# Kernel optimization log

Measured on AMD Instinct MI355X. Metric: run time of the kernel, lower is better.

The kernel has to match this reference:

```python
import jax, jax.numpy as jnp
import numpy as np

B, T, D, H = 4, 2048, 1024, 16
HD = D // H  # head_dim = 64

def setup_inputs() -> dict:
    key = jax.random.key(0)
    k1, k2, k3 = jax.random.split(key, 3)
    s = 1.0 / np.sqrt(D)
    x = jax.random.normal(k1, (B, T, D), dtype=jnp.float32)
    W_qkv = jax.random.normal(k2, (D, 3 * D), dtype=jnp.float32) * s
    W_proj = jax.random.normal(k3, (D, D), dtype=jnp.float32) * s
    return {"x": x, "W_qkv": W_qkv, "W_proj": W_proj}

def reference(x, W_qkv, W_proj):
    Bq, Tq, C = x.shape
    qkv = x @ W_qkv                                   # [B,T,3C]
    q, k, v = jnp.split(qkv, 3, axis=-1)
    def heads(t):  # [B,T,C] -> [B,H,T,HD]
        return t.reshape(Bq, Tq, H, HD).transpose(0, 2, 1, 3)
    q, k, v = heads(q), heads(k), heads(v)
    scale = 1.0 / np.sqrt(HD)
    att = jnp.einsum('bhqd,bhkd->bhqk', q, k) * scale  # [B,H,T,T]
    causal = jnp.tril(jnp.ones((Tq, Tq), dtype=bool))
    att = jnp.where(causal[None, None], att, -jnp.inf)
    att = jax.nn.softmax(att, axis=-1)
    y = jnp.einsum('bhqk,bhkd->bhqd', att, v)          # [B,H,T,HD]
    y = y.transpose(0, 2, 1, 3).reshape(Bq, Tq, C)
    return y @ W_proj
```

## Files before the change

kernel.cpp:

```cpp
#include <hip/hip_runtime.h>

typedef unsigned short ushort_t;
typedef __attribute__((ext_vector_type(8))) __bf16 bf16x8;
typedef __attribute__((ext_vector_type(4))) float f32x4;
typedef __attribute__((ext_vector_type(16))) float f32x16;
typedef __attribute__((ext_vector_type(4))) float float4v;
typedef __attribute__((ext_vector_type(8))) unsigned short ushort8v;
typedef __attribute__((ext_vector_type(4))) unsigned short ushort4v;
typedef __attribute__((ext_vector_type(4))) unsigned uint4v;

#define T_LEN 2048
#define D_DIM 1024
#define NHEAD 16
#define HDIM 64
#define BH 64
#define MROWS 8192
#define PERQKV ((size_t)BH * T_LEN * HDIM)

__device__ __forceinline__ ushort_t f2bf(float f) {
  unsigned u = __builtin_bit_cast(unsigned, f);
  u = (u + 0x7FFFu + ((u >> 16) & 1u)) >> 16;
  return (ushort_t)u;
}

__device__ __forceinline__ float fast_exp2(float x) {
  float r; asm("v_exp_f32 %0, %1" : "=v"(r) : "v"(x)); return r;
}
__device__ __forceinline__ float fast_rcp(float x) {
  float r; asm("v_rcp_f32 %0, %1" : "=v"(r) : "v"(x)); return r;
}

__device__ __forceinline__ void load_lds16(const ushort_t* g, ushort_t* l) {
  __builtin_amdgcn_global_load_lds((const __attribute__((address_space(1))) void*)g,
                                   (__attribute__((address_space(3))) void*)l, 16, 0, 0);
}

__global__ __launch_bounds__(256) void k_prep(const float* __restrict__ x,
                                              const float* __restrict__ Wqkv,
                                              const float* __restrict__ Wproj,
                                              ushort_t* __restrict__ xb,
                                              ushort_t* __restrict__ WqT,
                                              ushort_t* __restrict__ WpT) {
  __shared__ ushort_t tile[32][33];
  int bid = blockIdx.x, tid = threadIdx.x;
  if (bid < 8192) {
    int i = bid * 256 + tid;
    float4v v = ((const float4v*)x)[i];
    ushort4v o;
    o[0] = f2bf(v[0]); o[1] = f2bf(v[1]); o[2] = f2bf(v[2]); o[3] = f2bf(v[3]);
    ((ushort4v*)xb)[i] = o;
    return;
  }
  bid -= 8192;
  int bx = bid & 127, by = bid >> 7;
  const float* W; ushort_t* Wt; int C;
  if (bx < 96) { W = Wqkv; Wt = WqT; C = 3072; }
  else         { W = Wproj; Wt = WpT; C = 1024; bx -= 96; }
  const int R = 1024;
  int tx = tid & 31, ty = tid >> 5;
  int r0 = by << 5, c0 = bx << 5;
#pragma unroll
  for (int i = 0; i < 4; ++i) {
    int r = ty + i * 8;
    tile[r][tx] = f2bf(W[(size_t)(r0 + r) * C + c0 + tx]);
  }
  __syncthreads();
#pragma unroll
  for (int i = 0; i < 4; ++i) {
    int r = ty + i * 8;
    Wt[(size_t)(c0 + r) * R + r0 + tx] = tile[tx][r];
  }
}

template <int N, int K, int EPI>
__global__ __launch_bounds__(256) void k_gemm(const ushort_t* __restrict__ A,
                                              const ushort_t* __restrict__ Bt,
                                              ushort_t* __restrict__ O16,
                                              float* __restrict__ O32) {
  __shared__ __align__(16) ushort_t Atile[128 * 32];
  __shared__ __align__(16) ushort_t Btile[128 * 32];
  const int tid = threadIdx.x;
  const int lane = tid & 63, w = tid >> 6;
  const int g = lane >> 4, c = lane & 15;
  const int wm = w >> 1, wn = w & 1;
  const int m0 = blockIdx.y * 128, n0 = blockIdx.x * 128;

  f32x4 acc[4][4];
#pragma unroll
  for (int i = 0; i < 4; ++i)
#pragma unroll
    for (int j = 0; j < 4; ++j) acc[i][j] = (f32x4){0.f, 0.f, 0.f, 0.f};

  for (int k0 = 0; k0 < K; k0 += 32) {
    __syncthreads();
#pragma unroll
    for (int r = 0; r < 2; ++r) {
      int flat = r * 256 + tid;
      int row = flat >> 2, slot = flat & 3;
      int gsl = slot ^ (row & 3);
      load_lds16(A + (size_t)(m0 + row) * K + k0 + gsl * 8,
                 &Atile[(r * 256 + w * 64) * 8]);
      load_lds16(Bt + (size_t)(n0 + row) * K + k0 + gsl * 8,
                 &Btile[(r * 256 + w * 64) * 8]);
    }
    __syncthreads();

    bf16x8 af[4], bfr[4];
#pragma unroll
    for (int mi = 0; mi < 4; ++mi) {
      int row = wm * 64 + mi * 16 + c;
      int sl = g ^ (row & 3);
      af[mi] = *(const bf16x8*)&Atile[row * 32 + sl * 8];
    }
#pragma unroll
    for (int ni = 0; ni < 4; ++ni) {
      int row = wn * 64 + ni * 16 + c;
      int sl = g ^ (row & 3);
      bfr[ni] = *(const bf16x8*)&Btile[row * 32 + sl * 8];
    }
#pragma unroll
    for (int mi = 0; mi < 4; ++mi)
#pragma unroll
      for (int ni = 0; ni < 4; ++ni)
        acc[mi][ni] = __builtin_amdgcn_mfma_f32_16x16x32_bf16(af[mi], bfr[ni],
                                                              acc[mi][ni], 0, 0, 0);
  }

#pragma unroll
  for (int mi = 0; mi < 4; ++mi)
#pragma unroll
    for (int ni = 0; ni < 4; ++ni) {
      int n = n0 + wn * 64 + ni * 16 + c;
#pragma unroll
      for (int j = 0; j < 4; ++j) {
        int m = m0 + wm * 64 + mi * 16 + g * 4 + j;
        float v = acc[mi][ni][j];
        if constexpr (EPI == 0) {
          int which = n >> 10, hn = n & 1023;
          int h = hn >> 6, d = hn & 63;
          int b = m >> 11, t = m & 2047;
          if (which == 0) v *= 0.18033688f;
          O16[(size_t)which * PERQKV +
              (((size_t)(b * NHEAD + h) * T_LEN + t) * HDIM + d)] = f2bf(v);
        } else {
          O32[(size_t)m * N + n] = v;
        }
      }
    }
}

template <int NB_TILES, int EPI>
__global__ __launch_bounds__(512, 2) void k_gemm3(const ushort_t* __restrict__ A,
                                                  const ushort_t* __restrict__ Bt,
                                                  ushort_t* __restrict__ O16,
                                                  float* __restrict__ O32) {
  __shared__ __align__(16) ushort_t As[3][128 * 64];
  __shared__ __align__(16) ushort_t Bs[3][256 * 64];
  const int tid = threadIdx.x, lane = tid & 63, w = tid >> 6;
  const int g = lane >> 4, c = lane & 15;
  const int wm = w & 1, wn = w >> 1;
  const int nblk = 64 * NB_TILES;
  const int chunk = nblk >> 3;
  const int bid = blockIdx.x;
  const int logical = (bid & 7) * chunk + (bid >> 3);
  const int mb = logical & 63, nb = logical >> 6;
  const int m0 = mb * 128, n0 = nb * 256;

  const int srow = lane >> 3, sgran = lane & 7;

  auto stage = [&](int t, int buf) {
    const int k0 = t * 64;
#pragma unroll
    for (int l = 0; l < 2; ++l) {
      int r = w * 16 + l * 8 + srow;
      load_lds16(A + (size_t)(m0 + r) * 1024 + k0 + ((sgran ^ (r & 7)) << 3),
                 &As[buf][(w * 16 + l * 8) * 64]);
    }
#pragma unroll
    for (int l = 0; l < 4; ++l) {
      int r = w * 32 + l * 8 + srow;
      load_lds16(Bt + (size_t)(n0 + r) * 1024 + k0 + ((sgran ^ (r & 7)) << 3),
                 &Bs[buf][(w * 32 + l * 8) * 64]);
    }
  };

  f32x4 acc[4][4];
#pragma unroll
  for (int i = 0; i < 4; ++i)
#pragma unroll
    for (int j = 0; j < 4; ++j) acc[i][j] = (f32x4){0.f, 0.f, 0.f, 0.f};

  stage(0, 0);
  stage(1, 1);

  for (int t = 0; t < 16; ++t) {
    if (t < 15) asm volatile("s_waitcnt vmcnt(6)" ::: "memory");
    else        asm volatile("s_waitcnt vmcnt(0)" ::: "memory");
    __builtin_amdgcn_s_barrier();
    __builtin_amdgcn_sched_barrier(0);

    if (t + 2 < 16) stage(t + 2, (t + 2) % 3);

    const int cur = t % 3;
    const ushort_t* abuf = &As[cur][0];
    const ushort_t* bbuf = &Bs[cur][0];
#pragma unroll
    for (int kk = 0; kk < 2; ++kk) {
      bf16x8 af[4], bq[4];
#pragma unroll
      for (int fr = 0; fr < 4; ++fr) {
        int r = wm * 64 + fr * 16 + c;
        af[fr] = *(const bf16x8*)&abuf[r * 64 + (((kk * 4 + g) ^ (r & 7)) << 3)];
      }
#pragma unroll
      for (int fc = 0; fc < 4; ++fc) {
        int r = wn * 64 + fc * 16 + c;
        bq[fc] = *(const bf16x8*)&bbuf[r * 64 + (((kk * 4 + g) ^ (r & 7)) << 3)];
      }
      __builtin_amdgcn_s_setprio(1);
#pragma unroll
      for (int fr = 0; fr < 4; ++fr)
#pragma unroll
        for (int fc = 0; fc < 4; ++fc)
          acc[fr][fc] = __builtin_amdgcn_mfma_f32_16x16x32_bf16(af[fr], bq[fc],
                                                                acc[fr][fc], 0, 0, 0);
      __builtin_amdgcn_s_setprio(0);
    }
  }

#pragma unroll
  for (int fr = 0; fr < 4; ++fr)
#pragma unroll
    for (int fc = 0; fc < 4; ++fc) {
      int n = n0 + wn * 64 + fc * 16 + c;
#pragma unroll
      for (int j = 0; j < 4; ++j) {
        int m = m0 + wm * 64 + fr * 16 + g * 4 + j;
        float v = acc[fr][fc][j];
        if constexpr (EPI == 0) {
          int which = n >> 10, hn = n & 1023;
          int h = hn >> 6, d = hn & 63;
          int b = m >> 11, tt = m & 2047;
          if (which == 0) v *= 0.18033688f;
          O16[(size_t)which * PERQKV +
              (((size_t)(b * NHEAD + h) * T_LEN + tt) * HDIM + d)] = f2bf(v);
        } else {
          O32[(size_t)m * (64 * NB_TILES * 4) + n] = v;
        }
      }
    }
}

__global__ __launch_bounds__(128, 2) void k_attn(const ushort_t* __restrict__ Q,
                                                 const ushort_t* __restrict__ Kv,
                                                 const ushort_t* __restrict__ Vv,
                                                 ushort_t* __restrict__ Y) {
  __shared__ __align__(16) ushort_t Kt[2][64 * 64];
  __shared__ __align__(16) ushort_t Vt[2][64 * 64];

  const int bid = blockIdx.x;
  const int bh = (bid & 7) * 8 + ((bid >> 3) & 7);
  const int pairidx = bid >> 6;
  const int pA = 31 - pairidx, pB = pairidx;
  const int nktA = pA + 1;
  const int total = nktA + pB + 1;

  const int tid = threadIdx.x, lane = tid & 63, w = tid >> 6;
  const int hi = lane >> 5, lc = lane & 31;
  const size_t base = (size_t)bh * (T_LEN * HDIM);

  f32x16 z16;
#pragma unroll
  for (int i = 0; i < 16; ++i) z16[i] = 0.f;
  uint4v ow; ow[0] = ow[1] = ow[2] = ow[3] = 0x3F803F80u;
  const bf16x8 onesf = __builtin_bit_cast(bf16x8, ow);

  int q32 = pA * 64 + w * 32;
  bf16x8 qf[4];
#pragma unroll
  for (int st = 0; st < 4; ++st)
    qf[st] = *(const bf16x8*)(Q + base + (size_t)(q32 + lc) * HDIM + st * 16 + hi * 8);

  f32x16 o0, o1, ol;
#pragma unroll
  for (int i = 0; i < 16; ++i) { o0[i] = 0.f; o1[i] = 0.f; ol[i] = 0.f; }
  float mrun = 0.f;

  const int ksl = tid & 7, krow0 = tid >> 3;
  const int kpair = tid & 31, vk0 = 2 * kpair, vd0 = (tid >> 5) * 8;

  bf16x8 kreg[4];
  ushort8v vreg[4];
  auto stage_issue = [&](int kt) {
    const ushort_t* kb = Kv + base + (size_t)kt * 64 * HDIM;
    const ushort_t* vb = Vv + base + (size_t)kt * 64 * HDIM;
    vreg[0] = *(const ushort8v*)(vb + (size_t)vk0 * HDIM + vd0);
    vreg[1] = *(const ushort8v*)(vb + (size_t)(vk0 + 1) * HDIM + vd0);
    vreg[2] = *(const ushort8v*)(vb + (size_t)vk0 * HDIM + vd0 + 32);
    vreg[3] = *(const ushort8v*)(vb + (size_t)(vk0 + 1) * HDIM + vd0 + 32);
#pragma unroll
    for (int m = 0; m < 4; ++m)
      kreg[m] = *(const bf16x8*)(kb + (size_t)(krow0 + 16 * m) * HDIM + ksl * 8);
  };
  auto stage_write = [&](int buf) {
#pragma unroll
    for (int m = 0; m < 4; ++m) {
      int r = krow0 + 16 * m;
      *(bf16x8*)&Kt[buf][r * 64 + ((ksl ^ (r & 7)) << 3)] = kreg[m];
    }
    uint4v a0 = __builtin_bit_cast(uint4v, vreg[0]);
    uint4v a1 = __builtin_bit_cast(uint4v, vreg[1]);
    uint4v a2 = __builtin_bit_cast(uint4v, vreg[2]);
    uint4v a3 = __builtin_bit_cast(uint4v, vreg[3]);
#pragma unroll
    for (int i = 0; i < 4; ++i) {
      unsigned lo, hi2, lo2, hi3;
      asm("v_perm_b32 %0, %1, %2, %3" : "=v"(lo)  : "v"(a1[i]), "v"(a0[i]), "s"(0x05040100u));
      asm("v_perm_b32 %0, %1, %2, %3" : "=v"(hi2) : "v"(a1[i]), "v"(a0[i]), "s"(0x07060302u));
      asm("v_perm_b32 %0, %1, %2, %3" : "=v"(lo2) : "v"(a3[i]), "v"(a2[i]), "s"(0x05040100u));
      asm("v_perm_b32 %0, %1, %2, %3" : "=v"(hi3) : "v"(a3[i]), "v"(a2[i]), "s"(0x07060302u));
      int rd = vd0 + 2 * i;
      *(unsigned*)&Vt[buf][rd * 64 + (((kpair >> 2) ^ (rd & 7)) << 3) + 2 * (kpair & 3)] = lo;
      int rd1 = rd + 1;
      *(unsigned*)&Vt[buf][rd1 * 64 + (((kpair >> 2) ^ (rd1 & 7)) << 3) + 2 * (kpair & 3)] = hi2;
      int rd2 = rd + 32;
      *(unsigned*)&Vt[buf][rd2 * 64 + (((kpair >> 2) ^ (rd2 & 7)) << 3) + 2 * (kpair & 3)] = lo2;
      int rd3 = rd + 33;
      *(unsigned*)&Vt[buf][rd3 * 64 + (((kpair >> 2) ^ (rd3 & 7)) << 3) + 2 * (kpair & 3)] = hi3;
    }
  };

  const int b_ = bh >> 4, h_ = bh & 15;
  auto epilogue = [&]() {
#pragma unroll
    for (int r = 0; r < 16; ++r) {
      int cr = (r & 3) + 8 * (r >> 2) + 4 * hi;
      float iv = fast_rcp(ol[r]);
      size_t m = (size_t)b_ * T_LEN + q32 + cr;
      Y[m * D_DIM + h_ * HDIM + lc]      = f2bf(o0[r] * iv);
      Y[m * D_DIM + h_ * HDIM + 32 + lc] = f2bf(o1[r] * iv);
    }
  };

  stage_issue(0); stage_write(0);
  stage_issue(1);
  __syncthreads();

  for (int it = 0; it < total; ++it) {
    if (it == nktA) {
      epilogue();
      q32 = pB * 64 + w * 32;
#pragma unroll
      for (int st = 0; st < 4; ++st)
        qf[st] = *(const bf16x8*)(Q + base + (size_t)(q32 + lc) * HDIM + st * 16 + hi * 8);
#pragma unroll
      for (int i = 0; i < 16; ++i) { o0[i] = 0.f; o1[i] = 0.f; ol[i] = 0.f; }
      mrun = 0.f;
    }
    const int kt = (it < nktA) ? it : it - nktA;
    const int cur = it & 1;
    const ushort_t* kbuf = &Kt[cur][0];
    const ushort_t* vbuf = &Vt[cur][0];

    __builtin_amdgcn_s_setprio(1);
    bf16x8 kf0 = *(const bf16x8*)&kbuf[lc * 64 + ((hi ^ (lc & 7)) << 3)];
    f32x16 s0 = __builtin_amdgcn_mfma_f32_32x32x16_bf16(kf0, qf[0], z16, 0, 0, 0);
#pragma unroll
    for (int st = 1; st < 4; ++st) {
      bf16x8 kf = *(const bf16x8*)&kbuf[lc * 64 + (((2 * st + hi) ^ (lc & 7)) << 3)];
      s0 = __builtin_amdgcn_mfma_f32_32x32x16_bf16(kf, qf[st], s0, 0, 0, 0);
    }
    bf16x8 kg0 = *(const bf16x8*)&kbuf[(32 + lc) * 64 + ((hi ^ (lc & 7)) << 3)];
    f32x16 s1 = __builtin_amdgcn_mfma_f32_32x32x16_bf16(kg0, qf[0], z16, 0, 0, 0);
#pragma unroll
    for (int st = 1; st < 4; ++st) {
      bf16x8 kg = *(const bf16x8*)&kbuf[(32 + lc) * 64 + (((2 * st + hi) ^ (lc & 7)) << 3)];
      s1 = __builtin_amdgcn_mfma_f32_32x32x16_bf16(kg, qf[st], s1, 0, 0, 0);
    }
    __builtin_amdgcn_s_setprio(0);

    if (kt * 64 + 63 > q32) {
      const int q = q32 + lc;
#pragma unroll
      for (int r = 0; r < 16; ++r) {
        int cr = (r & 3) + 8 * (r >> 2) + 4 * hi;
        if (kt * 64 + cr > q)      s0[r] = -3.0e38f;
        if (kt * 64 + 32 + cr > q) s1[r] = -3.0e38f;
      }
    }

    float tm[8];
#pragma unroll
    for (int i = 0; i < 8; ++i) tm[i] = fmaxf(fmaxf(s0[i], s0[i + 8]), fmaxf(s1[i], s1[i + 8]));
#pragma unroll
    for (int i = 0; i < 4; ++i) tm[i] = fmaxf(tm[i], tm[i + 4]);
    float tmax = fmaxf(fmaxf(tm[0], tm[1]), fmaxf(tm[2], tm[3]));
    tmax = fmaxf(tmax, __shfl_xor(tmax, 32));

    if (!__all(tmax <= mrun + 11.0f)) {
      float mnew = fmaxf(mrun, tmax);
      float sc = fast_exp2(mrun - mnew);
      mrun = mnew;
#pragma unroll
      for (int r = 0; r < 16; ++r) {
        int cr = (r & 3) + 8 * (r >> 2) + 4 * hi;
        float scr = __shfl(sc, cr);
        o0[r] *= scr; o1[r] *= scr; ol[r] *= scr;
      }
    }

#pragma unroll
    for (int r = 0; r < 16; ++r) s0[r] = fast_exp2(s0[r] - mrun);
#pragma unroll
    for (int r = 0; r < 16; ++r) s1[r] = fast_exp2(s1[r] - mrun);

    unsigned wv[16];
#pragma unroll
    for (int i = 0; i < 8; ++i) {
      asm("v_cvt_pk_bf16_f32 %0, %1, %2" : "=v"(wv[i])     : "v"(s0[2 * i]), "v"(s0[2 * i + 1]));
      asm("v_cvt_pk_bf16_f32 %0, %1, %2" : "=v"(wv[8 + i]) : "v"(s1[2 * i]), "v"(s1[2 * i + 1]));
    }
    bf16x8 pf[4];
#pragma unroll
    for (int g4 = 0; g4 < 4; ++g4) {
      unsigned a0 = wv[4 * g4], a1 = wv[4 * g4 + 1];
      unsigned a2 = wv[4 * g4 + 2], a3 = wv[4 * g4 + 3];
      asm("v_permlane32_swap_b32 %0, %1" : "+v"(a0), "+v"(a2));
      asm("v_permlane32_swap_b32 %0, %1" : "+v"(a1), "+v"(a3));
      uint4v fw; fw[0] = a0; fw[1] = a1; fw[2] = a2; fw[3] = a3;
      pf[g4] = __builtin_bit_cast(bf16x8, fw);
    }

    if (it + 1 < total) stage_write((it + 1) & 1);

    __builtin_amdgcn_s_setprio(1);
#pragma unroll
    for (int km = 0; km < 4; ++km) {
      int gsl = ((2 * km + hi) ^ (lc & 7)) << 3;
      bf16x8 vb0 = *(const bf16x8*)&vbuf[lc * 64 + gsl];
      bf16x8 vb1 = *(const bf16x8*)&vbuf[(32 + lc) * 64 + gsl];
      o0 = __builtin_amdgcn_mfma_f32_32x32x16_bf16(pf[km], vb0, o0, 0, 0, 0);
      o1 = __builtin_amdgcn_mfma_f32_32x32x16_bf16(pf[km], vb1, o1, 0, 0, 0);
      ol = __builtin_amdgcn_mfma_f32_32x32x16_bf16(pf[km], onesf, ol, 0, 0, 0);
    }
    __builtin_amdgcn_s_setprio(0);

    if (it + 2 < total) {
      int itn = it + 2;
      stage_issue((itn < nktA) ? itn : itn - nktA);
    }
    __syncthreads();
  }

  epilogue();
}

extern "C" void kernel_launch(void* const* d_in, const int* in_sizes, int n_in,
                              void* d_out, int out_size, void* d_ws, size_t ws_size,
                              hipStream_t stream) {
  const float* x     = (const float*)d_in[0];
  const float* Wqkv  = (const float*)d_in[1];
  const float* Wproj = (const float*)d_in[2];
  float* out = (float*)d_out;
  ushort_t* ws = (ushort_t*)d_ws;

  ushort_t* Xb  = ws;
  ushort_t* WqT = Xb  + (size_t)MROWS * D_DIM;
  ushort_t* WpT = WqT + (size_t)3 * D_DIM * D_DIM;
  ushort_t* Qb  = WpT + (size_t)D_DIM * D_DIM;
  ushort_t* Kb  = Qb + PERQKV;
  ushort_t* Vb  = Kb + PERQKV;
  ushort_t* Yb  = Vb + PERQKV;

  k_prep<<<8192 + 4096, 256, 0, stream>>>(x, Wqkv, Wproj, Xb, WqT, WpT);
  k_gemm<3 * D_DIM, D_DIM, 0><<<dim3(3 * D_DIM / 128, MROWS / 128), 256, 0, stream>>>(Xb, WqT, Qb, nullptr);
  k_attn<<<1024, 128, 0, stream>>>(Qb, Kb, Vb, Yb);
  k_gemm3<4, 1><<<256, 512, 0, stream>>>(Yb, WpT, nullptr, out);
}
```

Before: 174.5 us.

## Process both causal query tiles concurrently in one block sharing K/V tiles

The attention block grows from two to four waves. Waves 0-1 handle the long query tile and waves 2-3 handle the short paired tile at the same time, instead of running the two tiles back to back. K/V tiles are staged into LDS once per iteration and shared by both tiles. Waves for the short tile skip compute once past their causal limit but keep helping with staging and barriers. A lookup table reorders which pair each block index gets, and launch bounds change to 256 threads, 4 blocks per CU. The intent is to cut the serial iteration count per block and the redundant K/V reloads, at the cost of idle waves late in the loop and higher register/LDS pressure per CU.

```diff
diff --git a/kernel.cpp b/kernel.cpp
--- a/kernel.cpp
+++ b/kernel.cpp
@@ -251,7 +251,7 @@
     }
 }
 
-__global__ __launch_bounds__(128, 2) void k_attn(const ushort_t* __restrict__ Q,
+__global__ __launch_bounds__(256, 4) void k_attn(const ushort_t* __restrict__ Q,
                                                  const ushort_t* __restrict__ Kv,
                                                  const ushort_t* __restrict__ Vv,
                                                  ushort_t* __restrict__ Y) {
@@ -260,10 +260,11 @@
 
   const int bid = blockIdx.x;
   const int bh = (bid & 7) * 8 + ((bid >> 3) & 7);
-  const int pairidx = bid >> 6;
-  const int pA = 31 - pairidx, pB = pairidx;
-  const int nktA = pA + 1;
-  const int total = nktA + pB + 1;
+  static const __device__ int PT[4][4] = {
+    {0, 15, 1, 14}, {2, 13, 3, 12}, {4, 11, 5, 10}, {6, 9, 7, 8}};
+  const int P = PT[(bid >> 6) & 3][bid >> 8];
+  const int pA = 31 - P, pB = P;
+  const int nkt = pA + 1;
 
   const int tid = threadIdx.x, lane = tid & 63, w = tid >> 6;
   const int hi = lane >> 5, lc = lane & 31;
@@ -275,7 +276,8 @@
   uint4v ow; ow[0] = ow[1] = ow[2] = ow[3] = 0x3F803F80u;
   const bf16x8 onesf = __builtin_bit_cast(bf16x8, ow);
 
-  int q32 = pA * 64 + w * 32;
+  const int myp = (w >> 1) ? pB : pA;
+  const int q32 = myp * 64 + (w & 1) * 32;
   bf16x8 qf[4];
 #pragma unroll
   for (int st = 0; st < 4; ++st)
@@ -289,170 +291,145 @@
   const int ksl = tid & 7, krow0 = tid >> 3;
   const int kpair = tid & 31, vk0 = 2 * kpair, vd0 = (tid >> 5) * 8;
 
-  bf16x8 kreg[4];
-  ushort8v vreg[4];
+  bf16x8 kreg[2];
+  ushort8v vreg[2];
   auto stage_issue = [&](int kt) {
     const ushort_t* kb = Kv + base + (size_t)kt * 64 * HDIM;
     const ushort_t* vb = Vv + base + (size_t)kt * 64 * HDIM;
     vreg[0] = *(const ushort8v*)(vb + (size_t)vk0 * HDIM + vd0);
     vreg[1] = *(const ushort8v*)(vb + (size_t)(vk0 + 1) * HDIM + vd0);
-    vreg[2] = *(const ushort8v*)(vb + (size_t)vk0 * HDIM + vd0 + 32);
-    vreg[3] = *(const ushort8v*)(vb + (size_t)(vk0 + 1) * HDIM + vd0 + 32);
-#pragma unroll
-    for (int m = 0; m < 4; ++m)
-      kreg[m] = *(const bf16x8*)(kb + (size_t)(krow0 + 16 * m) * HDIM + ksl * 8);
+    kreg[0] = *(const bf16x8*)(kb + (size_t)krow0 * HDIM + ksl * 8);
+    kreg[1] = *(const bf16x8*)(kb + (size_t)(krow0 + 32) * HDIM + ksl * 8);
   };
   auto stage_write = [&](int buf) {
 #pragma unroll
-    for (int m = 0; m < 4; ++m) {
-      int r = krow0 + 16 * m;
+    for (int m = 0; m < 2; ++m) {
+      int r = krow0 + 32 * m;
       *(bf16x8*)&Kt[buf][r * 64 + ((ksl ^ (r & 7)) << 3)] = kreg[m];
     }
     uint4v a0 = __builtin_bit_cast(uint4v, vreg[0]);
     uint4v a1 = __builtin_bit_cast(uint4v, vreg[1]);
-    uint4v a2 = __builtin_bit_cast(uint4v, vreg[2]);
-    uint4v a3 = __builtin_bit_cast(uint4v, vreg[3]);
 #pragma unroll
     for (int i = 0; i < 4; ++i) {
-      unsigned lo, hi2, lo2, hi3;
+      unsigned lo, hi2;
       asm("v_perm_b32 %0, %1, %2, %3" : "=v"(lo)  : "v"(a1[i]), "v"(a0[i]), "s"(0x05040100u));
       asm("v_perm_b32 %0, %1, %2, %3" : "=v"(hi2) : "v"(a1[i]), "v"(a0[i]), "s"(0x07060302u));
-      asm("v_perm_b32 %0, %1, %2, %3" : "=v"(lo2) : "v"(a3[i]), "v"(a2[i]), "s"(0x05040100u));
-      asm("v_perm_b32 %0, %1, %2, %3" : "=v"(hi3) : "v"(a3[i]), "v"(a2[i]), "s"(0x07060302u));
       int rd = vd0 + 2 * i;
       *(unsigned*)&Vt[buf][rd * 64 + (((kpair >> 2) ^ (rd & 7)) << 3) + 2 * (kpair & 3)] = lo;
       int rd1 = rd + 1;
       *(unsigned*)&Vt[buf][rd1 * 64 + (((kpair >> 2) ^ (rd1 & 7)) << 3) + 2 * (kpair & 3)] = hi2;
-      int rd2 = rd + 32;
-      *(unsigned*)&Vt[buf][rd2 * 64 + (((kpair >> 2) ^ (rd2 & 7)) << 3) + 2 * (kpair & 3)] = lo2;
-      int rd3 = rd + 33;
-      *(unsigned*)&Vt[buf][rd3 * 64 + (((kpair >> 2) ^ (rd3 & 7)) << 3) + 2 * (kpair & 3)] = hi3;
     }
   };
 
-  const int b_ = bh >> 4, h_ = bh & 15;
-  auto epilogue = [&]() {
-#pragma unroll
-    for (int r = 0; r < 16; ++r) {
-      int cr = (r & 3) + 8 * (r >> 2) + 4 * hi;
-      float iv = fast_rcp(ol[r]);
-      size_t m = (size_t)b_ * T_LEN + q32 + cr;
-      Y[m * D_DIM + h_ * HDIM + lc]      = f2bf(o0[r] * iv);
-      Y[m * D_DIM + h_ * HDIM + 32 + lc] = f2bf(o1[r] * iv);
-    }
-  };
-
   stage_issue(0); stage_write(0);
-  stage_issue(1);
+  if (nkt > 1) stage_issue(1);
   __syncthreads();
 
-  for (int it = 0; it < total; ++it) {
-    if (it == nktA) {
-      epilogue();
-      q32 = pB * 64 + w * 32;
-#pragma unroll
-      for (int st = 0; st < 4; ++st)
-        qf[st] = *(const bf16x8*)(Q + base + (size_t)(q32 + lc) * HDIM + st * 16 + hi * 8);
-#pragma unroll
-      for (int i = 0; i < 16; ++i) { o0[i] = 0.f; o1[i] = 0.f; ol[i] = 0.f; }
-      mrun = 0.f;
-    }
-    const int kt = (it < nktA) ? it : it - nktA;
-    const int cur = it & 1;
+  for (int kt = 0; kt < nkt; ++kt) {
+    const int cur = kt & 1;
     const ushort_t* kbuf = &Kt[cur][0];
     const ushort_t* vbuf = &Vt[cur][0];
 
-    __builtin_amdgcn_s_setprio(1);
-    bf16x8 kf0 = *(const bf16x8*)&kbuf[lc * 64 + ((hi ^ (lc & 7)) << 3)];
-    f32x16 s0 = __builtin_amdgcn_mfma_f32_32x32x16_bf16(kf0, qf[0], z16, 0, 0, 0);
-#pragma unroll
-    for (int st = 1; st < 4; ++st) {
-      bf16x8 kf = *(const bf16x8*)&kbuf[lc * 64 + (((2 * st + hi) ^ (lc & 7)) << 3)];
-      s0 = __builtin_amdgcn_mfma_f32_32x32x16_bf16(kf, qf[st], s0, 0, 0, 0);
-    }
-    bf16x8 kg0 = *(const bf16x8*)&kbuf[(32 + lc) * 64 + ((hi ^ (lc & 7)) << 3)];
-    f32x16 s1 = __builtin_amdgcn_mfma_f32_32x32x16_bf16(kg0, qf[0], z16, 0, 0, 0);
-#pragma unroll
-    for (int st = 1; st < 4; ++st) {
-      bf16x8 kg = *(const bf16x8*)&kbuf[(32 + lc) * 64 + (((2 * st + hi) ^ (lc & 7)) << 3)];
-      s1 = __builtin_amdgcn_mfma_f32_32x32x16_bf16(kg, qf[st], s1, 0, 0, 0);
-    }
-    __builtin_amdgcn_s_setprio(0);
-
-    if (kt * 64 + 63 > q32) {
-      const int q = q32 + lc;
-#pragma unroll
-      for (int r = 0; r < 16; ++r) {
-        int cr = (r & 3) + 8 * (r >> 2) + 4 * hi;
-        if (kt * 64 + cr > q)      s0[r] = -3.0e38f;
-        if (kt * 64 + 32 + cr > q) s1[r] = -3.0e38f;
-      }
-    }
-
-    float tm[8];
-#pragma unroll
-    for (int i = 0; i < 8; ++i) tm[i] = fmaxf(fmaxf(s0[i], s0[i + 8]), fmaxf(s1[i], s1[i + 8]));
-#pragma unroll
-    for (int i = 0; i < 4; ++i) tm[i] = fmaxf(tm[i], tm[i + 4]);
-    float tmax = fmaxf(fmaxf(tm[0], tm[1]), fmaxf(tm[2], tm[3]));
-    tmax = fmaxf(tmax, __shfl_xor(tmax, 32));
-
-    if (!__all(tmax <= mrun + 11.0f)) {
-      float mnew = fmaxf(mrun, tmax);
-      float sc = fast_exp2(mrun - mnew);
-      mrun = mnew;
-#pragma unroll
-      for (int r = 0; r < 16; ++r) {
-        int cr = (r & 3) + 8 * (r >> 2) + 4 * hi;
-        float scr = __shfl(sc, cr);
-        o0[r] *= scr; o1[r] *= scr; ol[r] *= scr;
-      }
-    }
-
-#pragma unroll
-    for (int r = 0; r < 16; ++r) s0[r] = fast_exp2(s0[r] - mrun);
-#pragma unroll
-    for (int r = 0; r < 16; ++r) s1[r] = fast_exp2(s1[r] - mrun);
-
-    unsigned wv[16];
-#pragma unroll
-    for (int i = 0; i < 8; ++i) {
-      asm("v_cvt_pk_bf16_f32 %0, %1, %2" : "=v"(wv[i])     : "v"(s0[2 * i]), "v"(s0[2 * i + 1]));
-      asm("v_cvt_pk_bf16_f32 %0, %1, %2" : "=v"(wv[8 + i]) : "v"(s1[2 * i]), "v"(s1[2 * i + 1]));
-    }
-    bf16x8 pf[4];
-#pragma unroll
-    for (int g4 = 0; g4 < 4; ++g4) {
-      unsigned a0 = wv[4 * g4], a1 = wv[4 * g4 + 1];
-      unsigned a2 = wv[4 * g4 + 2], a3 = wv[4 * g4 + 3];
-      asm("v_permlane32_swap_b32 %0, %1" : "+v"(a0), "+v"(a2));
-      asm("v_permlane32_swap_b32 %0, %1" : "+v"(a1), "+v"(a3));
-      uint4v fw; fw[0] = a0; fw[1] = a1; fw[2] = a2; fw[3] = a3;
-      pf[g4] = __builtin_bit_cast(bf16x8, fw);
-    }
-
-    if (it + 1 < total) stage_write((it + 1) & 1);
-
-    __builtin_amdgcn_s_setprio(1);
-#pragma unroll
-    for (int km = 0; km < 4; ++km) {
-      int gsl = ((2 * km + hi) ^ (lc & 7)) << 3;
-      bf16x8 vb0 = *(const bf16x8*)&vbuf[lc * 64 + gsl];
-      bf16x8 vb1 = *(const bf16x8*)&vbuf[(32 + lc) * 64 + gsl];
-      o0 = __builtin_amdgcn_mfma_f32_32x32x16_bf16(pf[km], vb0, o0, 0, 0, 0);
-      o1 = __builtin_amdgcn_mfma_f32_32x32x16_bf16(pf[km], vb1, o1, 0, 0, 0);
-      ol = __builtin_amdgcn_mfma_f32_32x32x16_bf16(pf[km], onesf, ol, 0, 0, 0);
-    }
-    __builtin_amdgcn_s_setprio(0);
-
-    if (it + 2 < total) {
-      int itn = it + 2;
-      stage_issue((itn < nktA) ? itn : itn - nktA);
-    }
+    if (kt * 64 <= q32 + 31) {
+      __builtin_amdgcn_s_setprio(1);
+      bf16x8 kf0 = *(const bf16x8*)&kbuf[lc * 64 + ((hi ^ (lc & 7)) << 3)];
+      f32x16 s0 = __builtin_amdgcn_mfma_f32_32x32x16_bf16(kf0, qf[0], z16, 0, 0, 0);
+#pragma unroll
+      for (int st = 1; st < 4; ++st) {
+        bf16x8 kf = *(const bf16x8*)&kbuf[lc * 64 + (((2 * st + hi) ^ (lc & 7)) << 3)];
+        s0 = __builtin_amdgcn_mfma_f32_32x32x16_bf16(kf, qf[st], s0, 0, 0, 0);
+      }
+      bf16x8 kg0 = *(const bf16x8*)&kbuf[(32 + lc) * 64 + ((hi ^ (lc & 7)) << 3)];
+      f32x16 s1 = __builtin_amdgcn_mfma_f32_32x32x16_bf16(kg0, qf[0], z16, 0, 0, 0);
+#pragma unroll
+      for (int st = 1; st < 4; ++st) {
+        bf16x8 kg = *(const bf16x8*)&kbuf[(32 + lc) * 64 + (((2 * st + hi) ^ (lc & 7)) << 3)];
+        s1 = __builtin_amdgcn_mfma_f32_32x32x16_bf16(kg, qf[st], s1, 0, 0, 0);
+      }
+      __builtin_amdgcn_s_setprio(0);
+
+      if (kt * 64 + 63 > q32) {
+        const int q = q32 + lc;
+#pragma unroll
+        for (int r = 0; r < 16; ++r) {
+          int cr = (r & 3) + 8 * (r >> 2) + 4 * hi;
+          if (kt * 64 + cr > q)      s0[r] = -3.0e38f;
+          if (kt * 64 + 32 + cr > q) s1[r] = -3.0e38f;
+        }
+      }
+
+      float tm[8];
+#pragma unroll
+      for (int i = 0; i < 8; ++i) tm[i] = fmaxf(fmaxf(s0[i], s0[i + 8]), fmaxf(s1[i], s1[i + 8]));
+#pragma unroll
+      for (int i = 0; i < 4; ++i) tm[i] = fmaxf(tm[i], tm[i + 4]);
+      float tmax = fmaxf(fmaxf(tm[0], tm[1]), fmaxf(tm[2], tm[3]));
+      tmax = fmaxf(tmax, __shfl_xor(tmax, 32));
+
+      if (!__all(tmax <= mrun + 11.0f)) {
+        float mnew = fmaxf(mrun, tmax);
+        float sc = fast_exp2(mrun - mnew);
+        mrun = mnew;
+#pragma unroll
+        for (int r = 0; r < 16; ++r) {
+          int cr = (r & 3) + 8 * (r >> 2) + 4 * hi;
+          float scr = __shfl(sc, cr);
+          o0[r] *= scr; o1[r] *= scr; ol[r] *= scr;
+        }
+      }
+
+#pragma unroll
+      for (int r = 0; r < 16; ++r) s0[r] = fast_exp2(s0[r] - mrun);
+#pragma unroll
+      for (int r = 0; r < 16; ++r) s1[r] = fast_exp2(s1[r] - mrun);
+
+      unsigned wv[16];
+#pragma unroll
+      for (int i = 0; i < 8; ++i) {
+        asm("v_cvt_pk_bf16_f32 %0, %1, %2" : "=v"(wv[i])     : "v"(s0[2 * i]), "v"(s0[2 * i + 1]));
+        asm("v_cvt_pk_bf16_f32 %0, %1, %2" : "=v"(wv[8 + i]) : "v"(s1[2 * i]), "v"(s1[2 * i + 1]));
+      }
+      bf16x8 pf[4];
+#pragma unroll
+      for (int g4 = 0; g4 < 4; ++g4) {
+        unsigned a0 = wv[4 * g4], a1 = wv[4 * g4 + 1];
+        unsigned a2 = wv[4 * g4 + 2], a3 = wv[4 * g4 + 3];
+        asm("v_permlane32_swap_b32 %0, %1" : "+v"(a0), "+v"(a2));
+        asm("v_permlane32_swap_b32 %0, %1" : "+v"(a1), "+v"(a3));
+        uint4v fw; fw[0] = a0; fw[1] = a1; fw[2] = a2; fw[3] = a3;
+        pf[g4] = __builtin_bit_cast(bf16x8, fw);
+      }
+
+      if (kt + 1 < nkt) stage_write((kt + 1) & 1);
+
+      __builtin_amdgcn_s_setprio(1);
+#pragma unroll
+      for (int km = 0; km < 4; ++km) {
+        int gsl = ((2 * km + hi) ^ (lc & 7)) << 3;
+        bf16x8 vb0 = *(const bf16x8*)&vbuf[lc * 64 + gsl];
+        bf16x8 vb1 = *(const bf16x8*)&vbuf[(32 + lc) * 64 + gsl];
+        o0 = __builtin_amdgcn_mfma_f32_32x32x16_bf16(pf[km], vb0, o0, 0, 0, 0);
+        o1 = __builtin_amdgcn_mfma_f32_32x32x16_bf16(pf[km], vb1, o1, 0, 0, 0);
+        ol = __builtin_amdgcn_mfma_f32_32x32x16_bf16(pf[km], onesf, ol, 0, 0, 0);
+      }
+      __builtin_amdgcn_s_setprio(0);
+    } else {
+      if (kt + 1 < nkt) stage_write((kt + 1) & 1);
+    }
+
+    if (kt + 2 < nkt) stage_issue(kt + 2);
     __syncthreads();
   }
 
-  epilogue();
+  const int b_ = bh >> 4, h_ = bh & 15;
+#pragma unroll
+  for (int r = 0; r < 16; ++r) {
+    int cr = (r & 3) + 8 * (r >> 2) + 4 * hi;
+    float iv = fast_rcp(ol[r]);
+    size_t m = (size_t)b_ * T_LEN + q32 + cr;
+    Y[m * D_DIM + h_ * HDIM + lc]      = f2bf(o0[r] * iv);
+    Y[m * D_DIM + h_ * HDIM + 32 + lc] = f2bf(o1[r] * iv);
+  }
 }
 
 extern "C" void kernel_launch(void* const* d_in, const int* in_sizes, int n_in,
@@ -474,6 +451,6 @@
 
   k_prep<<<8192 + 4096, 256, 0, stream>>>(x, Wqkv, Wproj, Xb, WqT, WpT);
   k_gemm<3 * D_DIM, D_DIM, 0><<<dim3(3 * D_DIM / 128, MROWS / 128), 256, 0, stream>>>(Xb, WqT, Qb, nullptr);
-  k_attn<<<1024, 128, 0, stream>>>(Qb, Kb, Vb, Yb);
+  k_attn<<<1024, 256, 0, stream>>>(Qb, Kb, Vb, Yb);
   k_gemm3<4, 1><<<256, 512, 0, stream>>>(Yb, WpT, nullptr, out);
 }
```

New measurement: 248.2 us. +42.2%, slower.
